# Kernel tuning notes

Hardware: AMD Instinct MI355X
Metric: run time of the kernel (lower is better)

The kernel has to match this reference:

```python
import jax, jax.numpy as jnp
import numpy as np
from jax import lax

H = 1024       # hidden_size
I = 1024       # intermediate_size (per expert)
E = 16         # num_experts
TOP_K = 4      # num_active_experts


def setup_inputs() -> dict:
    key = jax.random.key(0)
    ks = jax.random.split(key, 9)
    std_gate = 0.02 / (E ** 0.5)
    return {
        "hidden_states": jax.random.normal(ks[0], (1, 2048, H), jnp.float32),
        "gate_w": jax.random.normal(ks[1], (E, H), jnp.float32) * std_gate,
        "expert_bias": jnp.zeros((E,), jnp.float32),
        "w1": jax.random.normal(ks[2], (E, I, H), jnp.float32) * 0.02,
        "w2": jax.random.normal(ks[3], (E, H, I), jnp.float32) * 0.02,
        "w3": jax.random.normal(ks[4], (E, I, H), jnp.float32) * 0.02,
        "sw1": jax.random.normal(ks[5], (I, H), jnp.float32) * 0.02,
        "sw2": jax.random.normal(ks[6], (H, I), jnp.float32) * 0.02,
        "sw3": jax.random.normal(ks[7], (I, H), jnp.float32) * 0.02,
    }


def _swiglu(x, wg, wd, wu):
    # Swish(x W1^T) * (x W3^T) then W2^T
    return (jax.nn.silu(x @ wg.T) * (x @ wu.T)) @ wd.T


def reference(hidden_states, gate_w, expert_bias, w1, w2, w3, sw1, sw2, sw3):
    B, S, Hd = hidden_states.shape
    x = hidden_states.reshape(-1, Hd)              # [T, H]
    T = x.shape[0]

    # ---- Router ----
    router_logits = x @ gate_w.T                   # [T, E]
    biased = router_logits + expert_bias           # loss-free balancing bias
    _, sel = lax.top_k(biased, TOP_K)              # [T, K] indices from biased logits
    raw = jnp.take_along_axis(router_logits, sel, axis=-1)  # weights from UNbiased logits
    rw = jax.nn.softmax(raw.astype(jnp.float32), axis=-1).astype(x.dtype)  # [T, K]

    # Dense combine weights g[t, e] = routing weight if e selected else 0
    g = jnp.zeros((T, E), x.dtype).at[jnp.arange(T)[:, None], sel].add(rw)

    # ---- Routed experts (mathematically equal to grouped dispatch) ----
    routed = jnp.zeros_like(x)
    for e in range(E):  # fixed small expert loop
        routed = routed + g[:, e:e + 1] * _swiglu(x, w1[e], w2[e], w3[e])

    # ---- Shared expert ----
    shared = _swiglu(x, sw1, sw2, sw3)

    out = (shared + routed).reshape(B, S, Hd)      # dropout p=0 -> identity
    return out
```

## Files before the change

kernel.cpp:

```cpp
#include <hip/hip_runtime.h>
#include <cstddef>
#include <cstdint>

#define T_TOK 2048
#define HD 1024
#define ID 1024
#define NE 16
#define TOPK 4
#define BM 128
#define BN 128
#define BK 32
#define BM1 256
#define BN1 128
#define BK1 64
#define NK1 (HD / BK1)
#define MT_MAX 112
#define MT2_MAX 64
#define SLOT_CAP 16384

typedef float f32x4 __attribute__((ext_vector_type(4)));
typedef __bf16 bf16x8 __attribute__((ext_vector_type(8)));
typedef __bf16 bf16x4 __attribute__((ext_vector_type(4)));

#define WS_TILE_E 256
#define WS_TILE_E2 2048
#define WS_LOGITS 4096
#define WS_SLOT_TOK (WS_LOGITS + T_TOK * NE * 4)
#define WS_SLOT_W (WS_SLOT_TOK + SLOT_CAP * 4)
#define WS_H1 (WS_SLOT_W + SLOT_CAP * 4)
#define WS_XB (WS_H1 + (size_t)SLOT_CAP * ID * 2)
#define WS_W1B (WS_XB + (size_t)T_TOK * HD * 2)
#define EXSZ ((size_t)ID * HD)

__device__ __forceinline__ f32x4 mfma16(bf16x8 a, bf16x8 b, f32x4 c) {
  return __builtin_amdgcn_mfma_f32_16x16x32_bf16(a, b, c, 0, 0, 0);
}

__device__ __forceinline__ bf16x4 pack4(f32x4 a) {
  bf16x4 o;
  o[0] = (__bf16)a[0]; o[1] = (__bf16)a[1]; o[2] = (__bf16)a[2]; o[3] = (__bf16)a[3];
  return o;
}

__device__ __forceinline__ void gload16(const __bf16* g, __bf16* l) {
  __builtin_amdgcn_global_load_lds(
      (const __attribute__((address_space(1))) uint32_t*)g,
      (__attribute__((address_space(3))) uint32_t*)l, 16, 0, 0);
}

__device__ __forceinline__ void cvt_chunk(const float* __restrict__ src,
                                          __bf16* __restrict__ dst, size_t off,
                                          int tid) {
  const f32x4* p = (const f32x4*)src + off + tid;
  __bf16* q = dst + 4 * (off + tid);
  f32x4 v0 = __builtin_nontemporal_load(p);
  f32x4 v1 = __builtin_nontemporal_load(p + 256);
  f32x4 v2 = __builtin_nontemporal_load(p + 512);
  f32x4 v3 = __builtin_nontemporal_load(p + 768);
  f32x4 v4 = __builtin_nontemporal_load(p + 1024);
  f32x4 v5 = __builtin_nontemporal_load(p + 1280);
  f32x4 v6 = __builtin_nontemporal_load(p + 1536);
  f32x4 v7 = __builtin_nontemporal_load(p + 1792);
  *(bf16x4*)(q + 0 * 1024) = pack4(v0);
  *(bf16x4*)(q + 1 * 1024) = pack4(v1);
  *(bf16x4*)(q + 2 * 1024) = pack4(v2);
  *(bf16x4*)(q + 3 * 1024) = pack4(v3);
  *(bf16x4*)(q + 4 * 1024) = pack4(v4);
  *(bf16x4*)(q + 5 * 1024) = pack4(v5);
  *(bf16x4*)(q + 6 * 1024) = pack4(v6);
  *(bf16x4*)(q + 7 * 1024) = pack4(v7);
}

#define W4 ((size_t)1 << 22)
#define S4 ((size_t)1 << 18)
#define X4 ((size_t)1 << 19)
#define CVT4_TOTAL (2 * W4 + 2 * S4 + X4)
#define NCHUNK (CVT4_TOTAL / 2048)
#define CVT_GRID 2048
#define LOGITS_BLOCKS (T_TOK / 4)

__global__ __launch_bounds__(256) void fused_pre(
    const float* __restrict__ w1, const float* __restrict__ w3,
    const float* __restrict__ sw1, const float* __restrict__ sw3,
    const float* __restrict__ x, __bf16* __restrict__ w1b,
    __bf16* __restrict__ w3b, __bf16* __restrict__ xb,
    const float* __restrict__ gw, float* __restrict__ logits) {
  int tid = threadIdx.x;
  if ((int)blockIdx.x < LOGITS_BLOCKS) {
    int wv = tid >> 6;
    int lane = tid & 63;
    int tok = blockIdx.x * 4 + wv;
    int e = lane >> 2;
    int q = lane & 3;
    const float4* xr = (const float4*)(x + (size_t)tok * HD) + q * 64;
    const float4* wr = (const float4*)(gw + (size_t)e * HD) + q * 64;
    float s0 = 0.f, s1 = 0.f;
#pragma unroll 8
    for (int i = 0; i < 64; i += 2) {
      float4 a0 = xr[i], w0 = wr[i];
      float4 a1 = xr[i + 1], w1v = wr[i + 1];
      s0 += a0.x * w0.x + a0.y * w0.y + a0.z * w0.z + a0.w * w0.w;
      s1 += a1.x * w1v.x + a1.y * w1v.y + a1.z * w1v.z + a1.w * w1v.w;
    }
    float s = s0 + s1;
    s += __shfl_xor(s, 1);
    s += __shfl_xor(s, 2);
    if (q == 0) logits[(size_t)tok * NE + e] = s;
    return;
  }
  size_t b = blockIdx.x - LOGITS_BLOCKS;
  for (size_t c = b; c < NCHUNK; c += CVT_GRID) {
    size_t f = c * 2048;
    const float* src;
    __bf16* dst;
    size_t off;
    if (f < W4) { src = w1; dst = w1b; off = f; }
    else if (f < 2 * W4) { src = w3; dst = w3b; off = f - W4; }
    else if (f < 2 * W4 + S4) { src = sw1; dst = w1b + 16 * EXSZ; off = f - 2 * W4; }
    else if (f < 2 * W4 + 2 * S4) { src = sw3; dst = w3b + 16 * EXSZ; off = f - 2 * W4 - S4; }
    else { src = x; dst = xb; off = f - 2 * W4 - 2 * S4; }
    cvt_chunk(src, dst, off, tid);
  }
}

__global__ __launch_bounds__(256) void router_finish(
    const float* __restrict__ logits, const float* __restrict__ bias,
    int* __restrict__ tile_e, int* __restrict__ tile_e2,
    int* __restrict__ slot_tok, float* __restrict__ slot_w) {
  __shared__ int hist[NE];
  __shared__ int soff[NE + 1];
  __shared__ int fillp[NE];
  __shared__ unsigned lsel[T_TOK];
  __shared__ float4 lw4[T_TOK];

  int tid = threadIdx.x;
  if (tid < NE) { hist[tid] = 0; fillp[tid] = 0; }
  __syncthreads();

  float bb[NE];
#pragma unroll
  for (int e = 0; e < NE; ++e) bb[e] = bias[e];

  for (int j = 0; j < T_TOK / 256; ++j) {
    int t = tid + 256 * j;
    float lg[NE];
    const float4* lp = (const float4*)(logits + (size_t)t * NE);
#pragma unroll
    for (int q = 0; q < 4; ++q) {
      float4 v = lp[q];
      lg[4 * q] = v.x; lg[4 * q + 1] = v.y; lg[4 * q + 2] = v.z; lg[4 * q + 3] = v.w;
    }
    float b[NE];
#pragma unroll
    for (int e = 0; e < NE; ++e) b[e] = lg[e] + bb[e];

    int selk[TOPK];
    float raw[TOPK];
    unsigned used = 0;
#pragma unroll
    for (int k = 0; k < TOPK; ++k) {
      float best = -3.4e38f;
      int bi = 0;
#pragma unroll
      for (int e = 0; e < NE; ++e) {
        if (!((used >> e) & 1) && b[e] > best) { best = b[e]; bi = e; }
      }
      used |= (1u << bi);
      selk[k] = bi;
      raw[k] = lg[bi];
    }
    float m = raw[0];
#pragma unroll
    for (int k = 1; k < TOPK; ++k) m = fmaxf(m, raw[k]);
    float s = 0.f;
    float w[TOPK];
#pragma unroll
    for (int k = 0; k < TOPK; ++k) { w[k] = __expf(raw[k] - m); s += w[k]; }
    float inv = 1.f / s;
    lsel[t] = (unsigned)selk[0] | ((unsigned)selk[1] << 8) |
              ((unsigned)selk[2] << 16) | ((unsigned)selk[3] << 24);
    lw4[t] = make_float4(w[0] * inv, w[1] * inv, w[2] * inv, w[3] * inv);
#pragma unroll
    for (int k = 0; k < TOPK; ++k) atomicAdd(&hist[selk[k]], 1);
  }
  __syncthreads();

  if (tid == 0) {
    int o = 0;
    for (int e = 0; e < NE; ++e) { soff[e] = o; o += (hist[e] + BM1 - 1) & ~(BM1 - 1); }
    soff[NE] = o;
  }
  __syncthreads();
  int shared_base = soff[NE];
  int total = shared_base + T_TOK;
  for (int tt = tid; tt < MT_MAX; tt += 256) {
    int base = tt * BM;
    int ee = -1;
    if (base < shared_base) {
      ee = 0;
#pragma unroll
      for (int q = 1; q < NE; ++q) if (base >= soff[q]) ee = q;
    } else if (base < total) {
      ee = NE;
    }
    tile_e[tt] = ee;
  }
  for (int tt = tid; tt < MT2_MAX; tt += 256) {
    int base = tt * BM1;
    int ee = -1;
    if (base < shared_base) {
      ee = 0;
#pragma unroll
      for (int q = 1; q < NE; ++q) if (base >= soff[q]) ee = q;
    } else if (base < total) {
      ee = NE;
    }
    tile_e2[tt] = ee;
  }

  for (int j = 0; j < T_TOK / 256; ++j) {
    int t = tid + 256 * j;
    unsigned ps = lsel[t];
    float4 wv = lw4[t];
    int e0 = ps & 255, e1 = (ps >> 8) & 255, e2 = (ps >> 16) & 255, e3 = ps >> 24;
    int p0 = atomicAdd(&fillp[e0], 1);
    slot_tok[soff[e0] + p0] = t; slot_w[soff[e0] + p0] = wv.x;
    int p1 = atomicAdd(&fillp[e1], 1);
    slot_tok[soff[e1] + p1] = t; slot_w[soff[e1] + p1] = wv.y;
    int p2 = atomicAdd(&fillp[e2], 1);
    slot_tok[soff[e2] + p2] = t; slot_w[soff[e2] + p2] = wv.z;
    int p3 = atomicAdd(&fillp[e3], 1);
    slot_tok[soff[e3] + p3] = t; slot_w[soff[e3] + p3] = wv.w;
  }

  for (int s = tid; s < shared_base; s += 256) {
    int e = 0;
#pragma unroll
    for (int q = 1; q < NE; ++q) if (s >= soff[q]) e = q;
    if (s >= soff[e] + hist[e]) { slot_tok[s] = -1; slot_w[s] = 0.f; }
  }
  for (int s = shared_base + tid; s < total; s += 256) {
    slot_tok[s] = s - shared_base;
    slot_w[s] = 1.0f;
  }
}

#define P1_BLOCKS (8 * MT2_MAX)
#define W2CHUNKS ((int)((W4 + S4) / 4096))

__global__ __launch_bounds__(512, 2) void pass1_bf16(
    const __bf16* __restrict__ xb, const int* __restrict__ slot_tok,
    const int* __restrict__ tile_e2, const __bf16* __restrict__ w1b,
    const __bf16* __restrict__ w3b, __bf16* __restrict__ h1,
    const float* __restrict__ w2, const float* __restrict__ sw2,
    __bf16* __restrict__ w2b) {
  int tid = threadIdx.x;
  int bid = blockIdx.x;
  if (bid >= P1_BLOCKS) {
    size_t f = (size_t)(bid - P1_BLOCKS) * 4096;
    const float* src;
    __bf16* dst;
    size_t off;
    if (f < W4) { src = w2; dst = w2b; off = f; }
    else { src = sw2; dst = w2b + 16 * EXSZ; off = f - W4; }
    const f32x4* p = (const f32x4*)src + off + tid;
    __bf16* q = dst + 4 * (off + tid);
    f32x4 v0 = __builtin_nontemporal_load(p);
    f32x4 v1 = __builtin_nontemporal_load(p + 512);
    f32x4 v2 = __builtin_nontemporal_load(p + 1024);
    f32x4 v3 = __builtin_nontemporal_load(p + 1536);
    f32x4 v4 = __builtin_nontemporal_load(p + 2048);
    f32x4 v5 = __builtin_nontemporal_load(p + 2560);
    f32x4 v6 = __builtin_nontemporal_load(p + 3072);
    f32x4 v7 = __builtin_nontemporal_load(p + 3584);
    *(bf16x4*)(q + 0 * 2048) = pack4(v0);
    *(bf16x4*)(q + 1 * 2048) = pack4(v1);
    *(bf16x4*)(q + 2 * 2048) = pack4(v2);
    *(bf16x4*)(q + 3 * 2048) = pack4(v3);
    *(bf16x4*)(q + 4 * 2048) = pack4(v4);
    *(bf16x4*)(q + 5 * 2048) = pack4(v5);
    *(bf16x4*)(q + 6 * 2048) = pack4(v6);
    *(bf16x4*)(q + 7 * 2048) = pack4(v7);
    return;
  }
  int nt = bid & 7;
  int mt = bid >> 3;
  int e = tile_e2[mt];
  if (e < 0) return;
  int n0 = nt * BN1;
  int m0 = mt * BM1;

  const __bf16* wg = w1b + (size_t)e * EXSZ;
  const __bf16* wu = w3b + (size_t)e * EXSZ;

  __shared__ __align__(16) __bf16 As[2][BM1 * BK1];
  __shared__ __align__(16) __bf16 Bg[2][BN1 * BK1];
  __shared__ __align__(16) __bf16 Bu[2][BN1 * BK1];

  const __bf16* gA[4];
#pragma unroll
  for (int j = 0; j < 4; ++j) {
    int id = tid + j * 512;
    int r = id >> 3;
    int c = (id & 7) ^ (r & 7);
    int tok = slot_tok[m0 + r];
    if (tok < 0) tok = 0;
    gA[j] = xb + (size_t)tok * HD + c * 8;
  }
  const __bf16* gG[2];
  const __bf16* gU[2];
#pragma unroll
  for (int j = 0; j < 2; ++j) {
    int id = tid + j * 512;
    int r = id >> 3;
    int c = (id & 7) ^ (r & 7);
    gG[j] = wg + (size_t)(n0 + r) * HD + c * 8;
    gU[j] = wu + (size_t)(n0 + r) * HD + c * 8;
  }

  int wave = tid >> 6, lane = tid & 63;
  int wm = (wave >> 2) * 128;
  int wn = (wave & 3) * 32;
  int l16 = lane & 15, kch = lane >> 4;

  f32x4 accg[8][2] = {};
  f32x4 accu[8][2] = {};

  auto stage = [&](int B, int k0) {
#pragma unroll
    for (int j = 0; j < 4; ++j)
      gload16(gA[j] + k0, &As[B][(size_t)(tid + j * 512) * 8]);
#pragma unroll
    for (int j = 0; j < 2; ++j) {
      gload16(gG[j] + k0, &Bg[B][(size_t)(tid + j * 512) * 8]);
      gload16(gU[j] + k0, &Bu[B][(size_t)(tid + j * 512) * 8]);
    }
  };

#pragma unroll 1
  for (int k = 0; k < NK1; ++k) {
    int buf = k & 1;
    if (k == 0) stage(0, 0);
    if (k + 1 < NK1) {
      stage(buf ^ 1, (k + 1) * BK1);
      asm volatile("s_waitcnt vmcnt(8)" ::: "memory");
    } else {
      asm volatile("s_waitcnt vmcnt(0)" ::: "memory");
    }
    __builtin_amdgcn_s_barrier();
    __builtin_amdgcn_sched_barrier(0);

#pragma unroll
    for (int s = 0; s < 2; ++s) {
      bf16x8 af[8], gf[2], uf[2];
#pragma unroll
      for (int i = 0; i < 8; ++i) {
        int R = wm + i * 16 + l16;
        int c = s * 4 + kch;
        af[i] = *(const bf16x8*)(&As[buf][R * BK1 + ((c ^ (R & 7)) * 8)]);
      }
#pragma unroll
      for (int i = 0; i < 2; ++i) {
        int R = wn + i * 16 + l16;
        int c = s * 4 + kch;
        gf[i] = *(const bf16x8*)(&Bg[buf][R * BK1 + ((c ^ (R & 7)) * 8)]);
        uf[i] = *(const bf16x8*)(&Bu[buf][R * BK1 + ((c ^ (R & 7)) * 8)]);
      }
      asm volatile("s_waitcnt lgkmcnt(0)" ::: "memory");
      if (s == 1) __builtin_amdgcn_s_barrier();
      __builtin_amdgcn_sched_barrier(0);
#pragma unroll
      for (int mi = 0; mi < 8; ++mi)
#pragma unroll
        for (int ni = 0; ni < 2; ++ni) {
          accg[mi][ni] = mfma16(af[mi], gf[ni], accg[mi][ni]);
          accu[mi][ni] = mfma16(af[mi], uf[ni], accu[mi][ni]);
        }
    }
  }

#pragma unroll
  for (int mi = 0; mi < 8; ++mi) {
#pragma unroll
    for (int ni = 0; ni < 2; ++ni) {
#pragma unroll
      for (int j = 0; j < 4; ++j) {
        int row = m0 + wm + mi * 16 + kch * 4 + j;
        int col = n0 + wn + ni * 16 + l16;
        float g = accg[mi][ni][j];
        float u = accu[mi][ni][j];
        float hv = (g / (1.f + __expf(-g))) * u;
        h1[(size_t)row * ID + col] = (__bf16)hv;
      }
    }
  }
}

__global__ __launch_bounds__(256, 3) void pass2_bf16(
    const __bf16* __restrict__ h1, const int* __restrict__ slot_tok,
    const float* __restrict__ slot_w, const int* __restrict__ tile_e,
    const __bf16* __restrict__ w2b, float* __restrict__ out) {
  int mt = blockIdx.y;
  int e = tile_e[mt];
  if (e < 0) return;
  int n0 = blockIdx.x * BN;
  int m0 = mt * BM;

  const __bf16* wd = w2b + (size_t)e * EXSZ;

  __shared__ __align__(16) __bf16 As[2][BM * BK];
  __shared__ __align__(16) __bf16 Bs[2][BN * BK];

  int tid = threadIdx.x;
  int r0 = tid >> 2, r1 = r0 + 64;
  int c8 = ((tid & 3) ^ ((r0 >> 1) & 3)) * 8;
  const __bf16* gA0 = h1 + (size_t)(m0 + r0) * ID + c8;
  const __bf16* gA1 = h1 + (size_t)(m0 + r1) * ID + c8;
  const __bf16* gB0 = wd + (size_t)(n0 + r0) * ID + c8;
  const __bf16* gB1 = wd + (size_t)(n0 + r1) * ID + c8;

  int wave = tid >> 6, lane = tid & 63;
  int wm = (wave >> 1) * 64, wn = (wave & 1) * 64;
  int l16 = lane & 15, kch = lane >> 4;
  int kk8 = (kch ^ ((l16 >> 1) & 3)) * 8;

  f32x4 acc[4][4] = {};

  auto stage = [&](int B, int k0) {
    gload16(gA0 + k0, &As[B][(size_t)tid * 8]);
    gload16(gA1 + k0, &As[B][(size_t)(tid + 256) * 8]);
    gload16(gB0 + k0, &Bs[B][(size_t)tid * 8]);
    gload16(gB1 + k0, &Bs[B][(size_t)(tid + 256) * 8]);
  };
  auto body = [&](int B) {
    bf16x8 af[4], bf[4];
#pragma unroll
    for (int i = 0; i < 4; ++i) {
      af[i] = *(const bf16x8*)(&As[B][(wm + i * 16 + l16) * BK + kk8]);
      bf[i] = *(const bf16x8*)(&Bs[B][(wn + i * 16 + l16) * BK + kk8]);
    }
    asm volatile("s_waitcnt lgkmcnt(0)" ::: "memory");
    __builtin_amdgcn_s_barrier();
    __builtin_amdgcn_sched_barrier(0);
#pragma unroll
    for (int mi = 0; mi < 4; ++mi)
#pragma unroll
      for (int ni = 0; ni < 4; ++ni)
        acc[mi][ni] = mfma16(af[mi], bf[ni], acc[mi][ni]);
  };

  stage(0, 0);
#pragma unroll 1
  for (int k = 0; k < ID / BK - 1; ++k) {
    int cur = k & 1;
    stage(cur ^ 1, (k + 1) * BK);
    asm volatile("s_waitcnt vmcnt(4)" ::: "memory");
    __builtin_amdgcn_s_barrier();
    __builtin_amdgcn_sched_barrier(0);
    body(cur);
  }
  asm volatile("s_waitcnt vmcnt(0)" ::: "memory");
  __builtin_amdgcn_s_barrier();
  __builtin_amdgcn_sched_barrier(0);
  body((ID / BK - 1) & 1);

#pragma unroll
  for (int mi = 0; mi < 4; ++mi) {
#pragma unroll
    for (int j = 0; j < 4; ++j) {
      int row = m0 + wm + mi * 16 + kch * 4 + j;
      int token = slot_tok[row];
      if (token < 0) continue;
      float wgt = slot_w[row];
#pragma unroll
      for (int ni = 0; ni < 4; ++ni) {
        int col = n0 + wn + ni * 16 + l16;
        atomicAdd(out + (size_t)token * HD + col, wgt * acc[mi][ni][j]);
      }
    }
  }
}

extern "C" void kernel_launch(void* const* d_in, const int* in_sizes, int n_in,
                              void* d_out, int out_size, void* d_ws, size_t ws_size,
                              hipStream_t stream) {
  const float* x = (const float*)d_in[0];
  const float* gate_w = (const float*)d_in[1];
  const float* ebias = (const float*)d_in[2];
  const float* w1 = (const float*)d_in[3];
  const float* w2 = (const float*)d_in[4];
  const float* w3 = (const float*)d_in[5];
  const float* sw1 = (const float*)d_in[6];
  const float* sw2 = (const float*)d_in[7];
  const float* sw3 = (const float*)d_in[8];
  float* out = (float*)d_out;

  char* ws = (char*)d_ws;
  int* tile_e = (int*)(ws + WS_TILE_E);
  int* tile_e2 = (int*)(ws + WS_TILE_E2);
  float* logits = (float*)(ws + WS_LOGITS);
  int* slot_tok = (int*)(ws + WS_SLOT_TOK);
  float* slot_w = (float*)(ws + WS_SLOT_W);
  __bf16* h1 = (__bf16*)(ws + WS_H1);
  __bf16* xb = (__bf16*)(ws + WS_XB);
  __bf16* w1b = (__bf16*)(ws + WS_W1B);
  __bf16* w3b = w1b + 17 * EXSZ;
  __bf16* w2b = w3b + 17 * EXSZ;

  hipMemsetAsync(d_out, 0, (size_t)T_TOK * HD * sizeof(float), stream);

  fused_pre<<<LOGITS_BLOCKS + CVT_GRID, 256, 0, stream>>>(
      w1, w3, sw1, sw3, x, w1b, w3b, xb, gate_w, logits);
  router_finish<<<1, 256, 0, stream>>>(logits, ebias, tile_e, tile_e2, slot_tok,
                                       slot_w);

  pass1_bf16<<<P1_BLOCKS + W2CHUNKS, 512, 0, stream>>>(
      xb, slot_tok, tile_e2, w1b, w3b, h1, w2, sw2, w2b);
  pass2_bf16<<<dim3(HD / BN, MT_MAX), 256, 0, stream>>>(
      h1, slot_tok, slot_w, tile_e, w2b, out);
}
```

Measured before the change: 228.8 us.

## Retile down-projection GEMM to 256x128x64 tiles with 512-thread blocks

The second expert GEMM (h1 × W2) moves from 128x128x32 tiles with 256 threads to 256x128x64 tiles with 512 threads, matching the first pass. It reuses the 256-row expert tile map, so the separate 128-row tile map and its router code are dropped. Each k-step now runs two 32-wide sub-steps with an XOR-swizzled LDS layout and 8x2 MFMA accumulators per wave. Larger tiles raise arithmetic intensity and halve the barriers per K, but padding experts to 256 rows wastes more work and launches fewer, heavier blocks.

```diff
diff --git a/kernel.cpp b/kernel.cpp
--- a/kernel.cpp
+++ b/kernel.cpp
@@ -7,14 +7,10 @@
 #define ID 1024
 #define NE 16
 #define TOPK 4
-#define BM 128
-#define BN 128
-#define BK 32
 #define BM1 256
 #define BN1 128
 #define BK1 64
 #define NK1 (HD / BK1)
-#define MT_MAX 112
 #define MT2_MAX 64
 #define SLOT_CAP 16384
 
@@ -22,7 +18,6 @@
 typedef __bf16 bf16x8 __attribute__((ext_vector_type(8)));
 typedef __bf16 bf16x4 __attribute__((ext_vector_type(4)));
 
-#define WS_TILE_E 256
 #define WS_TILE_E2 2048
 #define WS_LOGITS 4096
 #define WS_SLOT_TOK (WS_LOGITS + T_TOK * NE * 4)
@@ -125,8 +120,8 @@
 
 __global__ __launch_bounds__(256) void router_finish(
     const float* __restrict__ logits, const float* __restrict__ bias,
-    int* __restrict__ tile_e, int* __restrict__ tile_e2,
-    int* __restrict__ slot_tok, float* __restrict__ slot_w) {
+    int* __restrict__ tile_e2, int* __restrict__ slot_tok,
+    float* __restrict__ slot_w) {
   __shared__ int hist[NE];
   __shared__ int soff[NE + 1];
   __shared__ int fillp[NE];
@@ -193,18 +188,6 @@
   __syncthreads();
   int shared_base = soff[NE];
   int total = shared_base + T_TOK;
-  for (int tt = tid; tt < MT_MAX; tt += 256) {
-    int base = tt * BM;
-    int ee = -1;
-    if (base < shared_base) {
-      ee = 0;
-#pragma unroll
-      for (int q = 1; q < NE; ++q) if (base >= soff[q]) ee = q;
-    } else if (base < total) {
-      ee = NE;
-    }
-    tile_e[tt] = ee;
-  }
   for (int tt = tid; tt < MT2_MAX; tt += 256) {
     int base = tt * BM1;
     int ee = -1;
@@ -396,76 +379,98 @@
   }
 }
 
-__global__ __launch_bounds__(256, 3) void pass2_bf16(
+__global__ __launch_bounds__(512, 2) void pass2_bf16(
     const __bf16* __restrict__ h1, const int* __restrict__ slot_tok,
-    const float* __restrict__ slot_w, const int* __restrict__ tile_e,
+    const float* __restrict__ slot_w, const int* __restrict__ tile_e2,
     const __bf16* __restrict__ w2b, float* __restrict__ out) {
-  int mt = blockIdx.y;
-  int e = tile_e[mt];
+  int tid = threadIdx.x;
+  int bid = blockIdx.x;
+  int nt = bid & 7;
+  int mt = bid >> 3;
+  int e = tile_e2[mt];
   if (e < 0) return;
-  int n0 = blockIdx.x * BN;
-  int m0 = mt * BM;
+  int n0 = nt * BN1;
+  int m0 = mt * BM1;
 
   const __bf16* wd = w2b + (size_t)e * EXSZ;
 
-  __shared__ __align__(16) __bf16 As[2][BM * BK];
-  __shared__ __align__(16) __bf16 Bs[2][BN * BK];
-
-  int tid = threadIdx.x;
-  int r0 = tid >> 2, r1 = r0 + 64;
-  int c8 = ((tid & 3) ^ ((r0 >> 1) & 3)) * 8;
-  const __bf16* gA0 = h1 + (size_t)(m0 + r0) * ID + c8;
-  const __bf16* gA1 = h1 + (size_t)(m0 + r1) * ID + c8;
-  const __bf16* gB0 = wd + (size_t)(n0 + r0) * ID + c8;
-  const __bf16* gB1 = wd + (size_t)(n0 + r1) * ID + c8;
+  __shared__ __align__(16) __bf16 As[2][BM1 * BK1];
+  __shared__ __align__(16) __bf16 Bs[2][BN1 * BK1];
+
+  const __bf16* gA[4];
+#pragma unroll
+  for (int j = 0; j < 4; ++j) {
+    int id = tid + j * 512;
+    int r = id >> 3;
+    int c = (id & 7) ^ (r & 7);
+    gA[j] = h1 + (size_t)(m0 + r) * ID + c * 8;
+  }
+  const __bf16* gB[2];
+#pragma unroll
+  for (int j = 0; j < 2; ++j) {
+    int id = tid + j * 512;
+    int r = id >> 3;
+    int c = (id & 7) ^ (r & 7);
+    gB[j] = wd + (size_t)(n0 + r) * ID + c * 8;
+  }
 
   int wave = tid >> 6, lane = tid & 63;
-  int wm = (wave >> 1) * 64, wn = (wave & 1) * 64;
+  int wm = (wave >> 2) * 128;
+  int wn = (wave & 3) * 32;
   int l16 = lane & 15, kch = lane >> 4;
-  int kk8 = (kch ^ ((l16 >> 1) & 3)) * 8;
-
-  f32x4 acc[4][4] = {};
+
+  f32x4 acc[8][2] = {};
 
   auto stage = [&](int B, int k0) {
-    gload16(gA0 + k0, &As[B][(size_t)tid * 8]);
-    gload16(gA1 + k0, &As[B][(size_t)(tid + 256) * 8]);
-    gload16(gB0 + k0, &Bs[B][(size_t)tid * 8]);
-    gload16(gB1 + k0, &Bs[B][(size_t)(tid + 256) * 8]);
+#pragma unroll
+    for (int j = 0; j < 4; ++j)
+      gload16(gA[j] + k0, &As[B][(size_t)(tid + j * 512) * 8]);
+#pragma unroll
+    for (int j = 0; j < 2; ++j)
+      gload16(gB[j] + k0, &Bs[B][(size_t)(tid + j * 512) * 8]);
   };
-  auto body = [&](int B) {
-    bf16x8 af[4], bf[4];
-#pragma unroll
-    for (int i = 0; i < 4; ++i) {
-      af[i] = *(const bf16x8*)(&As[B][(wm + i * 16 + l16) * BK + kk8]);
-      bf[i] = *(const bf16x8*)(&Bs[B][(wn + i * 16 + l16) * BK + kk8]);
-    }
-    asm volatile("s_waitcnt lgkmcnt(0)" ::: "memory");
+
+#pragma unroll 1
+  for (int k = 0; k < NK1; ++k) {
+    int buf = k & 1;
+    if (k == 0) stage(0, 0);
+    if (k + 1 < NK1) {
+      stage(buf ^ 1, (k + 1) * BK1);
+      asm volatile("s_waitcnt vmcnt(6)" ::: "memory");
+    } else {
+      asm volatile("s_waitcnt vmcnt(0)" ::: "memory");
+    }
     __builtin_amdgcn_s_barrier();
     __builtin_amdgcn_sched_barrier(0);
-#pragma unroll
-    for (int mi = 0; mi < 4; ++mi)
-#pragma unroll
-      for (int ni = 0; ni < 4; ++ni)
-        acc[mi][ni] = mfma16(af[mi], bf[ni], acc[mi][ni]);
-  };
-
-  stage(0, 0);
-#pragma unroll 1
-  for (int k = 0; k < ID / BK - 1; ++k) {
-    int cur = k & 1;
-    stage(cur ^ 1, (k + 1) * BK);
-    asm volatile("s_waitcnt vmcnt(4)" ::: "memory");
-    __builtin_amdgcn_s_barrier();
-    __builtin_amdgcn_sched_barrier(0);
-    body(cur);
-  }
-  asm volatile("s_waitcnt vmcnt(0)" ::: "memory");
-  __builtin_amdgcn_s_barrier();
-  __builtin_amdgcn_sched_barrier(0);
-  body((ID / BK - 1) & 1);
-
-#pragma unroll
-  for (int mi = 0; mi < 4; ++mi) {
+
+#pragma unroll
+    for (int s = 0; s < 2; ++s) {
+      bf16x8 af[8], bf[2];
+#pragma unroll
+      for (int i = 0; i < 8; ++i) {
+        int R = wm + i * 16 + l16;
+        int c = s * 4 + kch;
+        af[i] = *(const bf16x8*)(&As[buf][R * BK1 + ((c ^ (R & 7)) * 8)]);
+      }
+#pragma unroll
+      for (int i = 0; i < 2; ++i) {
+        int R = wn + i * 16 + l16;
+        int c = s * 4 + kch;
+        bf[i] = *(const bf16x8*)(&Bs[buf][R * BK1 + ((c ^ (R & 7)) * 8)]);
+      }
+      asm volatile("s_waitcnt lgkmcnt(0)" ::: "memory");
+      if (s == 1) __builtin_amdgcn_s_barrier();
+      __builtin_amdgcn_sched_barrier(0);
+#pragma unroll
+      for (int mi = 0; mi < 8; ++mi)
+#pragma unroll
+        for (int ni = 0; ni < 2; ++ni)
+          acc[mi][ni] = mfma16(af[mi], bf[ni], acc[mi][ni]);
+    }
+  }
+
+#pragma unroll
+  for (int mi = 0; mi < 8; ++mi) {
 #pragma unroll
     for (int j = 0; j < 4; ++j) {
       int row = m0 + wm + mi * 16 + kch * 4 + j;
@@ -473,7 +478,7 @@
       if (token < 0) continue;
       float wgt = slot_w[row];
 #pragma unroll
-      for (int ni = 0; ni < 4; ++ni) {
+      for (int ni = 0; ni < 2; ++ni) {
         int col = n0 + wn + ni * 16 + l16;
         atomicAdd(out + (size_t)token * HD + col, wgt * acc[mi][ni][j]);
       }
@@ -496,7 +501,6 @@
   float* out = (float*)d_out;
 
   char* ws = (char*)d_ws;
-  int* tile_e = (int*)(ws + WS_TILE_E);
   int* tile_e2 = (int*)(ws + WS_TILE_E2);
   float* logits = (float*)(ws + WS_LOGITS);
   int* slot_tok = (int*)(ws + WS_SLOT_TOK);
@@ -511,11 +515,10 @@
 
   fused_pre<<<LOGITS_BLOCKS + CVT_GRID, 256, 0, stream>>>(
       w1, w3, sw1, sw3, x, w1b, w3b, xb, gate_w, logits);
-  router_finish<<<1, 256, 0, stream>>>(logits, ebias, tile_e, tile_e2, slot_tok,
-                                       slot_w);
+  router_finish<<<1, 256, 0, stream>>>(logits, ebias, tile_e2, slot_tok, slot_w);
 
   pass1_bf16<<<P1_BLOCKS + W2CHUNKS, 512, 0, stream>>>(
       xb, slot_tok, tile_e2, w1b, w3b, h1, w2, sw2, w2b);
-  pass2_bf16<<<dim3(HD / BN, MT_MAX), 256, 0, stream>>>(
-      h1, slot_tok, slot_w, tile_e, w2b, out);
-}
+  pass2_bf16<<<8 * MT2_MAX, 512, 0, stream>>>(
+      h1, slot_tok, slot_w, tile_e2, w2b, out);
+}
```

Measured after the change: 259.3 us. 1.13x slower.

## Overlap single-block router with weight conversion in one launch

Applied to the files above, without the earlier changes.

The w1/w3/sw1/sw3 fp32-to-bf16 conversion moves out of the logits kernel and into the router kernel. Block 0 does the serial top-k routing while the other 2048 blocks convert weights. The logits kernel now only converts x alongside the logits. The goal is to hide the latency of the one-block router behind the bulk weight conversion instead of running it as a separate serialized launch. The router block uses a lot of shared memory, which may affect how the converter blocks get scheduled.

```diff
diff --git a/kernel.cpp b/kernel.cpp
--- a/kernel.cpp
+++ b/kernel.cpp
@@ -74,17 +74,12 @@
 #define W4 ((size_t)1 << 22)
 #define S4 ((size_t)1 << 18)
 #define X4 ((size_t)1 << 19)
-#define CVT4_TOTAL (2 * W4 + 2 * S4 + X4)
-#define NCHUNK (CVT4_TOTAL / 2048)
-#define CVT_GRID 2048
 #define LOGITS_BLOCKS (T_TOK / 4)
+#define XCHUNKS ((int)(X4 / 2048))
 
 __global__ __launch_bounds__(256) void fused_pre(
-    const float* __restrict__ w1, const float* __restrict__ w3,
-    const float* __restrict__ sw1, const float* __restrict__ sw3,
-    const float* __restrict__ x, __bf16* __restrict__ w1b,
-    __bf16* __restrict__ w3b, __bf16* __restrict__ xb,
-    const float* __restrict__ gw, float* __restrict__ logits) {
+    const float* __restrict__ x, const float* __restrict__ gw,
+    __bf16* __restrict__ xb, float* __restrict__ logits) {
   int tid = threadIdx.x;
   if ((int)blockIdx.x < LOGITS_BLOCKS) {
     int wv = tid >> 6;
@@ -108,32 +103,41 @@
     if (q == 0) logits[(size_t)tok * NE + e] = s;
     return;
   }
-  size_t b = blockIdx.x - LOGITS_BLOCKS;
-  for (size_t c = b; c < NCHUNK; c += CVT_GRID) {
-    size_t f = c * 2048;
-    const float* src;
-    __bf16* dst;
-    size_t off;
-    if (f < W4) { src = w1; dst = w1b; off = f; }
-    else if (f < 2 * W4) { src = w3; dst = w3b; off = f - W4; }
-    else if (f < 2 * W4 + S4) { src = sw1; dst = w1b + 16 * EXSZ; off = f - 2 * W4; }
-    else if (f < 2 * W4 + 2 * S4) { src = sw3; dst = w3b + 16 * EXSZ; off = f - 2 * W4 - S4; }
-    else { src = x; dst = xb; off = f - 2 * W4 - 2 * S4; }
-    cvt_chunk(src, dst, off, tid);
-  }
-}
-
-__global__ __launch_bounds__(256) void router_finish(
+  cvt_chunk(x, xb, (size_t)(blockIdx.x - LOGITS_BLOCKS) * 2048, tid);
+}
+
+#define RW_CHUNKS ((int)((2 * W4 + 2 * S4) / 2048))
+#define RC_GRID 2049
+
+__global__ __launch_bounds__(256) void router_cvt(
     const float* __restrict__ logits, const float* __restrict__ bias,
     int* __restrict__ tile_e, int* __restrict__ tile_e2,
-    int* __restrict__ slot_tok, float* __restrict__ slot_w) {
+    int* __restrict__ slot_tok, float* __restrict__ slot_w,
+    const float* __restrict__ w1, const float* __restrict__ w3,
+    const float* __restrict__ sw1, const float* __restrict__ sw3,
+    __bf16* __restrict__ w1b, __bf16* __restrict__ w3b) {
+  int tid = threadIdx.x;
+  if (blockIdx.x != 0) {
+    for (size_t c = blockIdx.x - 1; c < RW_CHUNKS; c += RC_GRID - 1) {
+      size_t f = c * 2048;
+      const float* src;
+      __bf16* dst;
+      size_t off;
+      if (f < W4) { src = w1; dst = w1b; off = f; }
+      else if (f < 2 * W4) { src = w3; dst = w3b; off = f - W4; }
+      else if (f < 2 * W4 + S4) { src = sw1; dst = w1b + 16 * EXSZ; off = f - 2 * W4; }
+      else { src = sw3; dst = w3b + 16 * EXSZ; off = f - 2 * W4 - S4; }
+      cvt_chunk(src, dst, off, tid);
+    }
+    return;
+  }
+
   __shared__ int hist[NE];
   __shared__ int soff[NE + 1];
   __shared__ int fillp[NE];
   __shared__ unsigned lsel[T_TOK];
   __shared__ float4 lw4[T_TOK];
 
-  int tid = threadIdx.x;
   if (tid < NE) { hist[tid] = 0; fillp[tid] = 0; }
   __syncthreads();
 
@@ -509,11 +513,10 @@
 
   hipMemsetAsync(d_out, 0, (size_t)T_TOK * HD * sizeof(float), stream);
 
-  fused_pre<<<LOGITS_BLOCKS + CVT_GRID, 256, 0, stream>>>(
-      w1, w3, sw1, sw3, x, w1b, w3b, xb, gate_w, logits);
-  router_finish<<<1, 256, 0, stream>>>(logits, ebias, tile_e, tile_e2, slot_tok,
-                                       slot_w);
-
+  fused_pre<<<LOGITS_BLOCKS + XCHUNKS, 256, 0, stream>>>(x, gate_w, xb, logits);
+  router_cvt<<<RC_GRID, 256, 0, stream>>>(logits, ebias, tile_e, tile_e2,
+                                          slot_tok, slot_w, w1, w3, sw1, sw3,
+                                          w1b, w3b);
   pass1_bf16<<<P1_BLOCKS + W2CHUNKS, 512, 0, stream>>>(
       xb, slot_tok, tile_e2, w1b, w3b, h1, w2, sw2, w2b);
   pass2_bf16<<<dim3(HD / BN, MT_MAX), 256, 0, stream>>>(
```

Measured after the change: 213.2 us. 6.8% less time.
